# Kernel tuning notes

Hardware: AMD Instinct MI355X
Metric: run time of the kernel (lower is better)

Reference implementation:

```python
import jax, jax.numpy as jnp
import numpy as np

EPS = 1e-08

def setup_inputs() -> dict:
    key = jax.random.key(0)
    k1, k2, k3 = jax.random.split(key, 3)
    shape = (4, 8, 2048, 64)  # [B, H, N, D]
    return {
        "q": jax.random.normal(k1, shape, dtype=jnp.float32),
        "k": jax.random.normal(k2, shape, dtype=jnp.float32),
        "v": jax.random.normal(k3, shape, dtype=jnp.float32),
    }

def reference(q, k, v):
    # Performer exp-kernel linear causal attention.
    d = q.shape[-1]
    data_normalizer = d ** (-0.25)
    # stabilization: q per-row max, k per-(seq,feature)-block max
    q = q - jnp.max(q, axis=-1, keepdims=True)
    k = k - jnp.max(k, axis=(-2, -1), keepdims=True)
    q = jnp.exp(data_normalizer * q) + EPS
    k = jnp.exp(data_normalizer * k) + EPS
    # denominator: q . cumsum_n(k)
    k_cumsum = jnp.cumsum(k, axis=-2) + EPS
    D_inv = 1.0 / jnp.einsum('bhnd,bhnd->bhn', q, k_cumsum)
    # causal numerator: out[n] = q[n] . cumsum_n(k[n] outer v[n])
    kv = jnp.cumsum(k[..., :, :, None] * v[..., :, None, :], axis=-3)  # [B,H,N,Dk,Dv]
    out = jnp.einsum('bhne,bhnef->bhnf', q, kv)
    return out * D_inv[..., None]
```

## Files before the change

### kernel.cpp

```cpp
#include <hip/hip_runtime.h>


#define NSEQ 2048
#define DD 64
#define CH 64
#define NC (NSEQ / CH)
#define BHN 32
#define NCHUNK (BHN * NC)
#define EPSF 1e-8f
#define NRM 0.35355339059327373f
#define C1 (NRM * 1.4426950408889634f)

typedef short bf16x8 __attribute__((ext_vector_type(8)));
typedef float f32x4 __attribute__((ext_vector_type(4)));

__device__ __forceinline__ unsigned short f2bf(float f) {
  union { float f; unsigned u; } c; c.f = f;
  unsigned u = c.u + 0x7fffu + ((c.u >> 16) & 1u);
  return (unsigned short)(u >> 16);
}
__device__ __forceinline__ float bf2f(unsigned short s) {
  union { unsigned u; float f; } c; c.u = ((unsigned)s) << 16;
  return c.f;
}

__global__ __launch_bounds__(256) void kA_partial(const float* __restrict__ kg,
                                                  const float* __restrict__ vg,
                                                  float* __restrict__ ksum,
                                                  unsigned short* __restrict__ kvws) {
  __shared__ __align__(16) unsigned short Kt[DD * 72];
  __shared__ __align__(16) unsigned short Vt[DD * 72];
  const int blk = blockIdx.x;
  const int t = threadIdx.x;
  const size_t base = (size_t)blk * (CH * DD);
  const float4* k4 = (const float4*)(kg + base);
  const float4* v4 = (const float4*)(vg + base);
  {
    const int j0 = (t >> 4) << 2;
    const int e4 = t & 15, e0 = e4 << 2;
    float ka[4][4], va[4][4];
#pragma unroll
    for (int jj = 0; jj < 4; ++jj) {
      float4 kk = k4[(j0 + jj) * 16 + e4];
      float4 vv = v4[(j0 + jj) * 16 + e4];
      ka[jj][0] = exp2f(kk.x * C1) + EPSF;
      ka[jj][1] = exp2f(kk.y * C1) + EPSF;
      ka[jj][2] = exp2f(kk.z * C1) + EPSF;
      ka[jj][3] = exp2f(kk.w * C1) + EPSF;
      va[jj][0] = vv.x; va[jj][1] = vv.y; va[jj][2] = vv.z; va[jj][3] = vv.w;
    }
#pragma unroll
    for (int i = 0; i < 4; ++i) {
      short4 wk, wv;
      wk.x = (short)f2bf(ka[0][i]); wk.y = (short)f2bf(ka[1][i]);
      wk.z = (short)f2bf(ka[2][i]); wk.w = (short)f2bf(ka[3][i]);
      wv.x = (short)f2bf(va[0][i]); wv.y = (short)f2bf(va[1][i]);
      wv.z = (short)f2bf(va[2][i]); wv.w = (short)f2bf(va[3][i]);
      *(short4*)&Kt[(e0 + i) * 72 + j0] = wk;
      *(short4*)&Vt[(e0 + i) * 72 + j0] = wv;
    }
  }
  __syncthreads();
  const int wr = t >> 6, l = t & 63, lg = l >> 4, lc = l & 15;
  bf16x8 a0 = *(const bf16x8*)&Kt[(wr * 16 + lc) * 72 + lg * 8];
  bf16x8 a1 = *(const bf16x8*)&Kt[(wr * 16 + lc) * 72 + 32 + lg * 8];
  float ks = 0.f;
#pragma unroll
  for (int i = 0; i < 8; ++i) ks += bf2f((unsigned short)a0[i]) + bf2f((unsigned short)a1[i]);
  ks += __shfl_xor(ks, 16, 64);
  ks += __shfl_xor(ks, 32, 64);
  if (lg == 0) ksum[(size_t)blk * DD + wr * 16 + lc] = ks;
  f32x4 acc[4];
#pragma unroll
  for (int ft = 0; ft < 4; ++ft) acc[ft] = (f32x4){0.f, 0.f, 0.f, 0.f};
#pragma unroll
  for (int ft = 0; ft < 4; ++ft) {
    bf16x8 b0 = *(const bf16x8*)&Vt[(ft * 16 + lc) * 72 + lg * 8];
    bf16x8 b1 = *(const bf16x8*)&Vt[(ft * 16 + lc) * 72 + 32 + lg * 8];
    acc[ft] = __builtin_amdgcn_mfma_f32_16x16x32_bf16(a0, b0, acc[ft], 0, 0, 0);
    acc[ft] = __builtin_amdgcn_mfma_f32_16x16x32_bf16(a1, b1, acc[ft], 0, 0, 0);
  }
  unsigned short* kvb = kvws + (size_t)blk * (DD * DD);
  const int ee0 = wr * 16 + lg * 4;
#pragma unroll
  for (int ft = 0; ft < 4; ++ft) {
    short4 w;
    w.x = (short)f2bf(acc[ft][0]);
    w.y = (short)f2bf(acc[ft][1]);
    w.z = (short)f2bf(acc[ft][2]);
    w.w = (short)f2bf(acc[ft][3]);
    *(short4*)&kvb[(ft * 16 + lc) * DD + ee0] = w;
  }
}

__global__ __launch_bounds__(256) void kB_out(const float* __restrict__ qg,
                                              const float* __restrict__ kg,
                                              const float* __restrict__ vg,
                                              const float* __restrict__ ksum,
                                              const unsigned short* __restrict__ kvws,
                                              float* __restrict__ out) {
  __shared__ __align__(16) unsigned short Kb[CH * 72];
  __shared__ __align__(16) unsigned short Vt[DD * 72];
  __shared__ __align__(16) unsigned short KVp[DD * 72];
  __shared__ __align__(16) unsigned short Sl[4][16 * 40];
  __shared__ float kspf[DD];
  const int blk = blockIdx.x;
  const int bh = blk >> 5, c = blk & 31;
  const int t = threadIdx.x;
  const size_t base = (size_t)blk * (CH * DD);
  const float4* k4 = (const float4*)(kg + base);
  const float4* v4 = (const float4*)(vg + base);
  {
    const int j0 = (t >> 4) << 2;
    const int e4 = t & 15, e0 = e4 << 2;
    float va[4][4];
#pragma unroll
    for (int jj = 0; jj < 4; ++jj) {
      float4 kk = k4[(j0 + jj) * 16 + e4];
      float4 vv = v4[(j0 + jj) * 16 + e4];
      short4 w;
      w.x = (short)f2bf(exp2f(kk.x * C1) + EPSF);
      w.y = (short)f2bf(exp2f(kk.y * C1) + EPSF);
      w.z = (short)f2bf(exp2f(kk.z * C1) + EPSF);
      w.w = (short)f2bf(exp2f(kk.w * C1) + EPSF);
      *(short4*)&Kb[(j0 + jj) * 72 + e0] = w;
      va[jj][0] = vv.x; va[jj][1] = vv.y; va[jj][2] = vv.z; va[jj][3] = vv.w;
    }
#pragma unroll
    for (int i = 0; i < 4; ++i) {
      short4 wv;
      wv.x = (short)f2bf(va[0][i]); wv.y = (short)f2bf(va[1][i]);
      wv.z = (short)f2bf(va[2][i]); wv.w = (short)f2bf(va[3][i]);
      *(short4*)&Vt[(e0 + i) * 72 + j0] = wv;
    }
  }
  {
    float pf[16];
#pragma unroll
    for (int i = 0; i < 16; ++i) pf[i] = 0.f;
    const unsigned short* kvbase =
        kvws + ((size_t)bh * NC) * (DD * DD) + (size_t)t * 16;
#pragma unroll
    for (int j0 = 0; j0 < NC; j0 += 8) {
      if (j0 >= c) break;
      bf16x8 x0[8], x1[8];
#pragma unroll
      for (int jj = 0; jj < 8; ++jj) {
        const unsigned short* p = kvbase + (size_t)(j0 + jj) * (DD * DD);
        x0[jj] = *(const bf16x8*)p;
        x1[jj] = *(const bf16x8*)(p + 8);
      }
#pragma unroll
      for (int jj = 0; jj < 8; ++jj) {
        float w = (j0 + jj < c) ? 1.f : 0.f;
#pragma unroll
        for (int i = 0; i < 8; ++i) {
          pf[i]     += w * bf2f((unsigned short)x0[jj][i]);
          pf[8 + i] += w * bf2f((unsigned short)x1[jj][i]);
        }
      }
    }
    bf16x8 w0, w1;
#pragma unroll
    for (int i = 0; i < 8; ++i) {
      w0[i] = (short)f2bf(pf[i]);
      w1[i] = (short)f2bf(pf[8 + i]);
    }
    unsigned short* kvrow = &KVp[(t >> 2) * 72 + (t & 3) * 16];
    *(bf16x8*)kvrow = w0;
    *(bf16x8*)(kvrow + 8) = w1;
  }
  if (t < DD) {
    float s = 0.f;
    const float* kp = ksum + ((size_t)bh * NC) * DD + t;
#pragma unroll
    for (int j = 0; j < NC - 1; ++j) {
      float x = kp[(size_t)j * DD];
      s += (j < c) ? x : 0.f;
    }
    kspf[t] = s;
  }
  const int wr = t >> 6, l = t & 63, lg = l >> 4, lc = l & 15;
  float qe[2][8];
  const float* qrow = qg + base + (size_t)(wr * 16 + lc) * DD;
#pragma unroll
  for (int kt = 0; kt < 2; ++kt) {
    float4 x = *(const float4*)(qrow + kt * 32 + lg * 8);
    float4 y = *(const float4*)(qrow + kt * 32 + lg * 8 + 4);
    qe[kt][0] = x.x; qe[kt][1] = x.y; qe[kt][2] = x.z; qe[kt][3] = x.w;
    qe[kt][4] = y.x; qe[kt][5] = y.y; qe[kt][6] = y.z; qe[kt][7] = y.w;
  }
  __syncthreads();

  bf16x8 qf[2];
  float dp = 0.f;
#pragma unroll
  for (int kt = 0; kt < 2; ++kt) {
    float4 s0 = *(const float4*)(kspf + kt * 32 + lg * 8);
    float4 s1 = *(const float4*)(kspf + kt * 32 + lg * 8 + 4);
    float ksv[8] = {s0.x, s0.y, s0.z, s0.w, s1.x, s1.y, s1.z, s1.w};
#pragma unroll
    for (int i = 0; i < 8; ++i) {
      float qv = exp2f(qe[kt][i] * C1) + EPSF;
      dp += qv * (ksv[i] + EPSF);
      qf[kt][i] = (short)f2bf(qv);
    }
  }
  dp += __shfl_xor(dp, 16, 64);
  dp += __shfl_xor(dp, 32, 64);

  f32x4 o[4];
#pragma unroll
  for (int ft = 0; ft < 4; ++ft) o[ft] = (f32x4){0.f, 0.f, 0.f, 0.f};

#pragma unroll
  for (int kt = 0; kt < 2; ++kt) {
#pragma unroll
    for (int ft = 0; ft < 4; ++ft) {
      bf16x8 b = *(const bf16x8*)&KVp[(ft * 16 + lc) * 72 + kt * 32 + lg * 8];
      o[ft] = __builtin_amdgcn_mfma_f32_16x16x32_bf16(qf[kt], b, o[ft], 0, 0, 0);
    }
  }

  float rs0 = 0.f, rs1 = 0.f, rs2 = 0.f, rs3 = 0.f;
  const int irow = wr * 16 + lg * 4;
  const int ng = (wr >> 1) + 1;
  for (int g = 0; g < ng; ++g) {
#pragma unroll
    for (int c2 = 0; c2 < 2; ++c2) {
      const int ct = 2 * g + c2;
      bf16x8 kb0 = *(const bf16x8*)&Kb[(ct * 16 + lc) * 72 + lg * 8];
      bf16x8 kb1 = *(const bf16x8*)&Kb[(ct * 16 + lc) * 72 + 32 + lg * 8];
      f32x4 s = (f32x4){0.f, 0.f, 0.f, 0.f};
      s = __builtin_amdgcn_mfma_f32_16x16x32_bf16(qf[0], kb0, s, 0, 0, 0);
      s = __builtin_amdgcn_mfma_f32_16x16x32_bf16(qf[1], kb1, s, 0, 0, 0);
      const int j = ct * 16 + lc;
      float v0 = (j <= irow + 0) ? s[0] : 0.f;
      float v1 = (j <= irow + 1) ? s[1] : 0.f;
      float v2 = (j <= irow + 2) ? s[2] : 0.f;
      float v3 = (j <= irow + 3) ? s[3] : 0.f;
      rs0 += v0; rs1 += v1; rs2 += v2; rs3 += v3;
      unsigned short* sl = &Sl[wr][0];
      sl[(lg * 4 + 0) * 40 + c2 * 16 + lc] = f2bf(v0);
      sl[(lg * 4 + 1) * 40 + c2 * 16 + lc] = f2bf(v1);
      sl[(lg * 4 + 2) * 40 + c2 * 16 + lc] = f2bf(v2);
      sl[(lg * 4 + 3) * 40 + c2 * 16 + lc] = f2bf(v3);
    }
    bf16x8 sa = *(const bf16x8*)&Sl[wr][lc * 40 + lg * 8];
#pragma unroll
    for (int ft = 0; ft < 4; ++ft) {
      bf16x8 vb = *(const bf16x8*)&Vt[(ft * 16 + lc) * 72 + g * 32 + lg * 8];
      o[ft] = __builtin_amdgcn_mfma_f32_16x16x32_bf16(sa, vb, o[ft], 0, 0, 0);
    }
  }
#pragma unroll
  for (int m = 1; m < 16; m <<= 1) {
    rs0 += __shfl_xor(rs0, m, 64);
    rs1 += __shfl_xor(rs1, m, 64);
    rs2 += __shfl_xor(rs2, m, 64);
    rs3 += __shfl_xor(rs3, m, 64);
  }
  float rsv[4] = {rs0, rs1, rs2, rs3};
  float* op = out + base;
#pragma unroll
  for (int reg = 0; reg < 4; ++reg) {
    float d = __shfl(dp, lg * 4 + reg, 64) + rsv[reg];
    float dinv = 1.0f / d;
#pragma unroll
    for (int ft = 0; ft < 4; ++ft) {
      op[(size_t)(irow + reg) * DD + ft * 16 + lc] = o[ft][reg] * dinv;
    }
  }
}

extern "C" void kernel_launch(void* const* d_in, const int* in_sizes, int n_in,
                              void* d_out, int out_size, void* d_ws, size_t ws_size,
                              hipStream_t stream) {
  const float* q = (const float*)d_in[0];
  const float* k = (const float*)d_in[1];
  const float* v = (const float*)d_in[2];
  float* out = (float*)d_out;
  float* ksum = (float*)d_ws;
  unsigned short* kvws = (unsigned short*)(ksum + (size_t)NCHUNK * DD);

  hipLaunchKernelGGL(kA_partial, dim3(NCHUNK), dim3(256), 0, stream,
                     k, v, ksum, kvws);
  hipLaunchKernelGGL(kB_out, dim3(NCHUNK), dim3(256), 0, stream,
                     q, k, v, ksum, kvws, out);
}
```

Baseline: 112.8 us.

## Replace per-chunk prefix re-summation with a separate exclusive scan kernel

Before, each output block summed all preceding chunks' KV states and k-sums itself, which is quadratic in chunk count and causes heavy redundant global reads. A new middle kernel now runs an in-place exclusive scan over the per-chunk KV (bf16 pairs) and k-sum workspaces. The output kernel then reads its own prefix state directly from global memory, with no shared-memory staging. This adds a third launch and an extra read-write pass over the workspace, and the scan accumulates in fp32 but stores each prefix back as bf16.

```diff
diff --git a/kernel.cpp b/kernel.cpp
--- a/kernel.cpp
+++ b/kernel.cpp
@@ -24,7 +24,7 @@
   return c.f;
 }
 
-__global__ __launch_bounds__(256) void kA_partial(const float* __restrict__ kg,
+__global__ __launch_bounds__(256) void k1_partial(const float* __restrict__ kg,
                                                   const float* __restrict__ vg,
                                                   float* __restrict__ ksum,
                                                   unsigned short* __restrict__ kvws) {
@@ -93,7 +93,39 @@
   }
 }
 
-__global__ __launch_bounds__(256) void kB_out(const float* __restrict__ qg,
+__global__ __launch_bounds__(256) void k2_scan(float* __restrict__ ksum,
+                                               unsigned short* __restrict__ kvws) {
+  const int blk = blockIdx.x;
+  const int t = threadIdx.x;
+  if (blk < 256) {
+    const int bh = blk >> 3;
+    const int col = (blk & 7) * 256 + t;
+    unsigned* p = (unsigned*)kvws + (size_t)bh * NC * 2048 + col;
+    unsigned x[NC];
+#pragma unroll
+    for (int c = 0; c < NC; ++c) x[c] = p[(size_t)c * 2048];
+    float a0 = 0.f, a1 = 0.f;
+#pragma unroll
+    for (int c = 0; c < NC; ++c) {
+      float x0 = bf2f((unsigned short)(x[c] & 0xffffu));
+      float x1 = bf2f((unsigned short)(x[c] >> 16));
+      p[(size_t)c * 2048] = (unsigned)f2bf(a0) | ((unsigned)f2bf(a1) << 16);
+      a0 += x0; a1 += x1;
+    }
+  } else {
+    const int gid = (blk - 256) * 256 + t;
+    const int bh = gid >> 6, e = gid & 63;
+    float* pk = ksum + (size_t)bh * NC * DD + e;
+    float x[NC];
+#pragma unroll
+    for (int c = 0; c < NC; ++c) x[c] = pk[(size_t)c * DD];
+    float run = 0.f;
+#pragma unroll
+    for (int c = 0; c < NC; ++c) { pk[(size_t)c * DD] = run; run += x[c]; }
+  }
+}
+
+__global__ __launch_bounds__(256) void k3_out(const float* __restrict__ qg,
                                               const float* __restrict__ kg,
                                               const float* __restrict__ vg,
                                               const float* __restrict__ ksum,
@@ -101,11 +133,8 @@
                                               float* __restrict__ out) {
   __shared__ __align__(16) unsigned short Kb[CH * 72];
   __shared__ __align__(16) unsigned short Vt[DD * 72];
-  __shared__ __align__(16) unsigned short KVp[DD * 72];
   __shared__ __align__(16) unsigned short Sl[4][16 * 40];
-  __shared__ float kspf[DD];
   const int blk = blockIdx.x;
-  const int bh = blk >> 5, c = blk & 31;
   const int t = threadIdx.x;
   const size_t base = (size_t)blk * (CH * DD);
   const float4* k4 = (const float4*)(kg + base);
@@ -134,52 +163,6 @@
       *(short4*)&Vt[(e0 + i) * 72 + j0] = wv;
     }
   }
-  {
-    float pf[16];
-#pragma unroll
-    for (int i = 0; i < 16; ++i) pf[i] = 0.f;
-    const unsigned short* kvbase =
-        kvws + ((size_t)bh * NC) * (DD * DD) + (size_t)t * 16;
-#pragma unroll
-    for (int j0 = 0; j0 < NC; j0 += 8) {
-      if (j0 >= c) break;
-      bf16x8 x0[8], x1[8];
-#pragma unroll
-      for (int jj = 0; jj < 8; ++jj) {
-        const unsigned short* p = kvbase + (size_t)(j0 + jj) * (DD * DD);
-        x0[jj] = *(const bf16x8*)p;
-        x1[jj] = *(const bf16x8*)(p + 8);
-      }
-#pragma unroll
-      for (int jj = 0; jj < 8; ++jj) {
-        float w = (j0 + jj < c) ? 1.f : 0.f;
-#pragma unroll
-        for (int i = 0; i < 8; ++i) {
-          pf[i]     += w * bf2f((unsigned short)x0[jj][i]);
-          pf[8 + i] += w * bf2f((unsigned short)x1[jj][i]);
-        }
-      }
-    }
-    bf16x8 w0, w1;
-#pragma unroll
-    for (int i = 0; i < 8; ++i) {
-      w0[i] = (short)f2bf(pf[i]);
-      w1[i] = (short)f2bf(pf[8 + i]);
-    }
-    unsigned short* kvrow = &KVp[(t >> 2) * 72 + (t & 3) * 16];
-    *(bf16x8*)kvrow = w0;
-    *(bf16x8*)(kvrow + 8) = w1;
-  }
-  if (t < DD) {
-    float s = 0.f;
-    const float* kp = ksum + ((size_t)bh * NC) * DD + t;
-#pragma unroll
-    for (int j = 0; j < NC - 1; ++j) {
-      float x = kp[(size_t)j * DD];
-      s += (j < c) ? x : 0.f;
-    }
-    kspf[t] = s;
-  }
   const int wr = t >> 6, l = t & 63, lg = l >> 4, lc = l & 15;
   float qe[2][8];
   const float* qrow = qg + base + (size_t)(wr * 16 + lc) * DD;
@@ -190,14 +173,13 @@
     qe[kt][0] = x.x; qe[kt][1] = x.y; qe[kt][2] = x.z; qe[kt][3] = x.w;
     qe[kt][4] = y.x; qe[kt][5] = y.y; qe[kt][6] = y.z; qe[kt][7] = y.w;
   }
-  __syncthreads();
-
   bf16x8 qf[2];
   float dp = 0.f;
+  const float* ksp = ksum + (size_t)blk * DD;
 #pragma unroll
   for (int kt = 0; kt < 2; ++kt) {
-    float4 s0 = *(const float4*)(kspf + kt * 32 + lg * 8);
-    float4 s1 = *(const float4*)(kspf + kt * 32 + lg * 8 + 4);
+    float4 s0 = *(const float4*)(ksp + kt * 32 + lg * 8);
+    float4 s1 = *(const float4*)(ksp + kt * 32 + lg * 8 + 4);
     float ksv[8] = {s0.x, s0.y, s0.z, s0.w, s1.x, s1.y, s1.z, s1.w};
 #pragma unroll
     for (int i = 0; i < 8; ++i) {
@@ -208,16 +190,18 @@
   }
   dp += __shfl_xor(dp, 16, 64);
   dp += __shfl_xor(dp, 32, 64);
+  __syncthreads();
 
   f32x4 o[4];
 #pragma unroll
   for (int ft = 0; ft < 4; ++ft) o[ft] = (f32x4){0.f, 0.f, 0.f, 0.f};
 
+  const unsigned short* kvb = kvws + (size_t)blk * (DD * DD);
 #pragma unroll
   for (int kt = 0; kt < 2; ++kt) {
 #pragma unroll
     for (int ft = 0; ft < 4; ++ft) {
-      bf16x8 b = *(const bf16x8*)&KVp[(ft * 16 + lc) * 72 + kt * 32 + lg * 8];
+      bf16x8 b = *(const bf16x8*)(kvb + (ft * 16 + lc) * DD + kt * 32 + lg * 8);
       o[ft] = __builtin_amdgcn_mfma_f32_16x16x32_bf16(qf[kt], b, o[ft], 0, 0, 0);
     }
   }
@@ -283,8 +267,9 @@
   float* ksum = (float*)d_ws;
   unsigned short* kvws = (unsigned short*)(ksum + (size_t)NCHUNK * DD);
 
-  hipLaunchKernelGGL(kA_partial, dim3(NCHUNK), dim3(256), 0, stream,
+  hipLaunchKernelGGL(k1_partial, dim3(NCHUNK), dim3(256), 0, stream,
                      k, v, ksum, kvws);
-  hipLaunchKernelGGL(kB_out, dim3(NCHUNK), dim3(256), 0, stream,
+  hipLaunchKernelGGL(k2_scan, dim3(264), dim3(256), 0, stream, ksum, kvws);
+  hipLaunchKernelGGL(k3_out, dim3(NCHUNK), dim3(256), 0, stream,
                      q, k, v, ksum, kvws, out);
 }
```

After: 106.9 us. 5.3% less time.
